# Optimization experiments

Measured on AMD Instinct MI355X. Metric: run time of the kernel, lower is better.

Reference implementation:

```python
import jax, jax.numpy as jnp
import numpy as np
import math

B, H, S, D = 2, 16, 2048, 128
COEFF = 2.0  # layer_number


def setup_inputs() -> dict:
    key = jax.random.key(0)
    kq, kk, kv = jax.random.split(key, 3)
    return {
        "query_layer": jax.random.normal(kq, (B, H, S, D), dtype=jnp.float32),
        "key_layer": jax.random.normal(kk, (B, H, S, D), dtype=jnp.float32),
        "value_layer": jax.random.normal(kv, (B, H, S, D), dtype=jnp.float32),
    }


def reference(query_layer, key_layer, value_layer):
    b, h, sq, d = query_layer.shape
    sk = key_layer.shape[2]
    norm_factor = math.sqrt(d) * COEFF
    # raw scores [b,h,sq,sk]; divide by sqrt(d)*coeff, cast fp32, multiply by coeff
    scores = jnp.einsum("bhqd,bhkd->bhqk", query_layer, key_layer) / norm_factor
    scores = scores.astype(jnp.float32) * COEFF
    # causal mask (sq == sk path with attention_mask=None)
    causal = jnp.tril(jnp.ones((sq, sk), dtype=bool))
    scores = jnp.where(causal, scores, jnp.float32(-jnp.inf))
    probs = jax.nn.softmax(scores, axis=-1).astype(value_layer.dtype)
    # dropout p=0.0 -> identity
    ctx = jnp.einsum("bhqk,bhkd->bhqd", probs, value_layer)
    # [b,h,sq,d] -> [b,sq,h*d]
    return ctx.transpose(0, 2, 1, 3).reshape(b, sq, h * d)
```

## Files before the change

### kernel.cpp

```cpp
#include <hip/hip_runtime.h>
#include <hip/hip_bf16.h>
#include <math.h>

#define NB 2
#define NH 16
#define NS 2048
#define ND 128

typedef __bf16 bf16x8 __attribute__((ext_vector_type(8)));
typedef __bf16 bf16x4 __attribute__((ext_vector_type(4)));
typedef float f32x4 __attribute__((ext_vector_type(4)));

#define KTILE 64
#define KSTR 136
#define VSTR 72
#define PSTR 72


__global__ __launch_bounds__(256, 2)
void fa_fwd(const float* __restrict__ Qg_, const float* __restrict__ Kg_,
            const float* __restrict__ Vg_, float* __restrict__ Out)
{
    __shared__ __bf16 Kl[KTILE][KSTR];
    __shared__ __bf16 Vt[ND + 16][VSTR];
    __shared__ __bf16 Pl[4][16][PSTR];

    const int tid  = threadIdx.x;
    const int w    = tid >> 6;
    const int lane = tid & 63;
    const int quad = lane >> 4;
    const int l15  = lane & 15;

    const int pr = blockIdx.x >> 5;
    const int bh = blockIdx.x & 31;
    const int b  = bh >> 4;
    const int h  = bh & 15;
    const int qtA = 31 - pr, qtB = pr;
    const int ntA = qtA + 1;
    const int total = ntA + qtB + 1;

    const float* Qg = Qg_ + (size_t)bh * NS * ND;
    const float* Kg = Kg_ + (size_t)bh * NS * ND;
    const float* Vg = Vg_ + (size_t)bh * NS * ND;

    for (int i = tid; i < 16*VSTR; i += 256) {
        int r = i / VSTR, c = i - r*VSTR;
        Vt[ND + r][c] = (r == 0) ? (__bf16)1.0f : (__bf16)0.0f;
    }

    const float CSC = 0.08838834764831845f * 1.4426950408889634f;

    bf16x8 qfA[4], qfB[4];
    const int qA = qtA * 64, qB = qtB * 64;
    {
        const float* qp = Qg + (size_t)(qA + 16*w + l15) * ND + quad*8;
        #pragma unroll
        for (int ks = 0; ks < 4; ++ks) {
            float4 a = *(const float4*)(qp + ks*32);
            float4 c = *(const float4*)(qp + ks*32 + 4);
            bf16x8 f;
            f[0]=(__bf16)(a.x*CSC); f[1]=(__bf16)(a.y*CSC); f[2]=(__bf16)(a.z*CSC); f[3]=(__bf16)(a.w*CSC);
            f[4]=(__bf16)(c.x*CSC); f[5]=(__bf16)(c.y*CSC); f[6]=(__bf16)(c.z*CSC); f[7]=(__bf16)(c.w*CSC);
            qfA[ks] = f;
        }
        const float* qp2 = Qg + (size_t)(qB + 16*w + l15) * ND + quad*8;
        #pragma unroll
        for (int ks = 0; ks < 4; ++ks) {
            float4 a = *(const float4*)(qp2 + ks*32);
            float4 c = *(const float4*)(qp2 + ks*32 + 4);
            bf16x8 f;
            f[0]=(__bf16)(a.x*CSC); f[1]=(__bf16)(a.y*CSC); f[2]=(__bf16)(a.z*CSC); f[3]=(__bf16)(a.w*CSC);
            f[4]=(__bf16)(c.x*CSC); f[5]=(__bf16)(c.y*CSC); f[6]=(__bf16)(c.z*CSC); f[7]=(__bf16)(c.w*CSC);
            qfB[ks] = f;
        }
    }
    bf16x8 qcur[4];
    #pragma unroll
    for (int ks = 0; ks < 4; ++ks) qcur[ks] = qfA[ks];

    f32x4 O[9];
    #pragma unroll
    for (int dt = 0; dt < 9; ++dt)
        #pragma unroll
        for (int r = 0; r < 4; ++r) O[dt][r] = 0.0f;

    float4 kp[8];
    float  vp[32];
    const int vc = tid & 127;
    const int vh = tid >> 7;

    {
        #pragma unroll
        for (int i = 0; i < 8; ++i)
            kp[i] = *(const float4*)(Kg + ((i*256 + tid) << 2));
        const float* vs = Vg + (size_t)(vh*32) * ND + vc;
        #pragma unroll
        for (int i = 0; i < 32; ++i) vp[i] = vs[i*ND];
    }

    for (int t = 0; t < total; ++t) {
        const int phase = (t >= ntA);
        const int jt  = phase ? t - ntA : t;
        const int kv0 = jt * KTILE;
        __syncthreads();

        #pragma unroll
        for (int i = 0; i < 8; ++i) {
            int idx = (i*256 + tid) << 2;
            int r = idx >> 7, c = idx & 127;
            bf16x4 f; f[0]=(__bf16)kp[i].x; f[1]=(__bf16)kp[i].y; f[2]=(__bf16)kp[i].z; f[3]=(__bf16)kp[i].w;
            *(bf16x4*)&Kl[r][c] = f;
        }
        #pragma unroll
        for (int g = 0; g < 4; ++g) {
            bf16x8 f;
            #pragma unroll
            for (int j = 0; j < 8; ++j) f[j] = (__bf16)vp[g*8 + j];
            *(bf16x8*)&Vt[vc][vh*32 + g*8] = f;
        }

        if (t + 1 < total) {
            const int jt2 = (t + 1 >= ntA) ? t + 1 - ntA : t + 1;
            const int kv1 = jt2 * KTILE;
            const float* ks2 = Kg + (size_t)kv1 * ND;
            #pragma unroll
            for (int i = 0; i < 8; ++i)
                kp[i] = *(const float4*)(ks2 + ((i*256 + tid) << 2));
            const float* vs = Vg + (size_t)(kv1 + vh*32) * ND + vc;
            #pragma unroll
            for (int i = 0; i < 32; ++i) vp[i] = vs[i*ND];
        }

        __syncthreads();

        if (t == ntA) {
            #pragma unroll
            for (int r = 0; r < 4; ++r) {
                float lsum = __shfl(O[8][r], lane & 48, 64);
                float inv = 1.0f / lsum;
                int q = qA + 16*w + quad*4 + r;
                float* op = Out + ((size_t)(b*NS + q)) * (NH*ND) + h*ND + l15;
                #pragma unroll
                for (int dt = 0; dt < 8; ++dt)
                    op[dt*16] = O[dt][r] * inv;
            }
            #pragma unroll
            for (int dt = 0; dt < 9; ++dt)
                #pragma unroll
                for (int r = 0; r < 4; ++r) O[dt][r] = 0.0f;
            #pragma unroll
            for (int ks = 0; ks < 4; ++ks) qcur[ks] = qfB[ks];
        }

        const int qb  = (phase ? qB : qA) + 16*w;
        const bool diag = (jt == (phase ? qtB : qtA));

        f32x4 Sf[4];
        #pragma unroll
        for (int n = 0; n < 4; ++n)
            #pragma unroll
            for (int r = 0; r < 4; ++r) Sf[n][r] = 0.0f;
        #pragma unroll
        for (int ks = 0; ks < 4; ++ks) {
            bf16x8 bf[4];
            #pragma unroll
            for (int n = 0; n < 4; ++n)
                bf[n] = *(const bf16x8*)&Kl[n*16 + l15][ks*32 + quad*8];
            #pragma unroll
            for (int n = 0; n < 4; ++n)
                Sf[n] = __builtin_amdgcn_mfma_f32_16x16x32_bf16(qcur[ks], bf[n], Sf[n], 0, 0, 0);
        }

        #pragma unroll
        for (int n = 0; n < 4; ++n) {
            const int kg = kv0 + n*16 + l15;
            #pragma unroll
            for (int r = 0; r < 4; ++r) {
                float tv = Sf[n][r];
                if (diag) {
                    int qg = qb + quad*4 + r;
                    if (kg > qg) tv = -INFINITY;
                }
                Pl[w][r*4 + quad][n*16 + l15] = (__bf16)exp2f(tv);
            }
        }

        #pragma unroll
        for (int ks = 0; ks < 2; ++ks) {
            bf16x8 af = *(const bf16x8*)&Pl[w][((l15 & 3) << 2) | (l15 >> 2)][ks*32 + quad*8];
            #pragma unroll
            for (int dt = 0; dt < 9; ++dt) {
                bf16x8 vf = *(const bf16x8*)&Vt[dt*16 + l15][ks*32 + quad*8];
                O[dt] = __builtin_amdgcn_mfma_f32_16x16x32_bf16(af, vf, O[dt], 0, 0, 0);
            }
        }
    }

    #pragma unroll
    for (int r = 0; r < 4; ++r) {
        float lsum = __shfl(O[8][r], lane & 48, 64);
        float inv = 1.0f / lsum;
        int q = qB + 16*w + quad*4 + r;
        float* op = Out + ((size_t)(b*NS + q)) * (NH*ND) + h*ND + l15;
        #pragma unroll
        for (int dt = 0; dt < 8; ++dt)
            op[dt*16] = O[dt][r] * inv;
    }
}

extern "C" void kernel_launch(void* const* d_in, const int* in_sizes, int n_in,
                              void* d_out, int out_size, void* d_ws, size_t ws_size,
                              hipStream_t stream) {
    const float* Q = (const float*)d_in[0];
    const float* K = (const float*)d_in[1];
    const float* V = (const float*)d_in[2];
    float* Out = (float*)d_out;
    dim3 grid(512);
    fa_fwd<<<grid, dim3(256), 0, stream>>>(Q, K, V, Out);
}
```

Baseline: 202.4 us.

## Pre-convert K/V to swizzled bf16 tiles and stream via async LDS loads

A new prep kernel converts K and V to bf16 once, writing per-tile XOR-swizzled layouts, with V stored transposed, into the workspace. The attention kernel then double-buffers those tiles into LDS with global_load_lds direct copies instead of register-staged fp32 loads and in-kernel conversion. It also swaps the MFMA operand order so P lands in LDS without a transpose, and replaces the ones-column row-sum trick with a register accumulator reduced by shuffles. This removes repeated fp32 K/V conversion per query tile and frees the extra MFMA column, at the cost of an extra kernel launch and a workspace round trip.

```diff
diff --git a/kernel.cpp b/kernel.cpp
--- a/kernel.cpp
+++ b/kernel.cpp
@@ -11,19 +11,52 @@
 typedef __bf16 bf16x4 __attribute__((ext_vector_type(4)));
 typedef float f32x4 __attribute__((ext_vector_type(4)));
 
-#define KTILE 64
-#define KSTR 136
-#define VSTR 72
-#define PSTR 72
-
+__global__ __launch_bounds__(256)
+void prep(const float* __restrict__ K, const float* __restrict__ V,
+          char* __restrict__ Kb, char* __restrict__ Vb)
+{
+    int g = blockIdx.x * 256 + threadIdx.x;
+    if (g < (1 << 20)) {
+        const int c8 = g & 15;
+        const int row = g >> 4;
+        const int s = row & 2047, bh = row >> 11;
+        const int jt = s >> 6, r = s & 63;
+        const float* src = K + ((size_t)row << 7) + (c8 << 3);
+        float4 a = *(const float4*)src;
+        float4 c = *(const float4*)(src + 4);
+        bf16x8 o;
+        o[0]=(__bf16)a.x; o[1]=(__bf16)a.y; o[2]=(__bf16)a.z; o[3]=(__bf16)a.w;
+        o[4]=(__bf16)c.x; o[5]=(__bf16)c.y; o[6]=(__bf16)c.z; o[7]=(__bf16)c.w;
+        *(bf16x8*)(Kb + (((size_t)(bh*32 + jt)) << 14) + r*256 + ((c8 ^ (r & 7)) << 4)) = o;
+    } else {
+        g -= (1 << 20);
+        const int t   = g >> 10;
+        const int off = g & 1023;
+        const int d = off >> 3, sl = off & 7;
+        const int g8 = sl ^ (d & 7);
+        const int bh = t >> 5, jt = t & 31;
+        const float* src = V + (((size_t)(bh*2048 + jt*64 + g8*8)) << 7) + d;
+        bf16x8 o;
+        #pragma unroll
+        for (int j = 0; j < 8; ++j) o[j] = (__bf16)src[(size_t)j << 7];
+        *(bf16x8*)(Vb + (((size_t)t) << 14) + d*128 + (sl << 4)) = o;
+    }
+}
+
+__device__ __forceinline__ void gld16(void* lds, const void* gsrc)
+{
+    __builtin_amdgcn_global_load_lds(
+        (const __attribute__((address_space(1))) void*)gsrc,
+        (__attribute__((address_space(3))) void*)lds, 16, 0, 0);
+}
 
 __global__ __launch_bounds__(256, 2)
-void fa_fwd(const float* __restrict__ Qg_, const float* __restrict__ Kg_,
-            const float* __restrict__ Vg_, float* __restrict__ Out)
+void fa_fwd(const float* __restrict__ Qg_, const char* __restrict__ Kb,
+            const char* __restrict__ Vb, float* __restrict__ Out)
 {
-    __shared__ __bf16 Kl[KTILE][KSTR];
-    __shared__ __bf16 Vt[ND + 16][VSTR];
-    __shared__ __bf16 Pl[4][16][PSTR];
+    __shared__ __bf16 Kl[2][8192];
+    __shared__ __bf16 Vl[2][8192];
+    __shared__ __bf16 Pl[4][1024];
 
     const int tid  = threadIdx.x;
     const int w    = tid >> 6;
@@ -33,27 +66,23 @@
 
     const int pr = blockIdx.x >> 5;
     const int bh = blockIdx.x & 31;
-    const int b  = bh >> 4;
-    const int h  = bh & 15;
+    const int b  = bh >> 4, h = bh & 15;
     const int qtA = 31 - pr, qtB = pr;
     const int ntA = qtA + 1;
     const int total = ntA + qtB + 1;
+    const int qA = qtA * 64, qB = qtB * 64;
 
     const float* Qg = Qg_ + (size_t)bh * NS * ND;
-    const float* Kg = Kg_ + (size_t)bh * NS * ND;
-    const float* Vg = Vg_ + (size_t)bh * NS * ND;
-
-    for (int i = tid; i < 16*VSTR; i += 256) {
-        int r = i / VSTR, c = i - r*VSTR;
-        Vt[ND + r][c] = (r == 0) ? (__bf16)1.0f : (__bf16)0.0f;
-    }
+    const char*  Kt = Kb + ((size_t)bh << 19);
+    const char*  Vt = Vb + ((size_t)bh << 19);
+
+    const int xo = (l15 & 7) << 4;
 
     const float CSC = 0.08838834764831845f * 1.4426950408889634f;
-
-    bf16x8 qfA[4], qfB[4];
-    const int qA = qtA * 64, qB = qtB * 64;
+    bf16x8 qfA[4], qfB[4], qcur[4];
     {
-        const float* qp = Qg + (size_t)(qA + 16*w + l15) * ND + quad*8;
+        const float* qp  = Qg + (size_t)(qA + 16*w + l15) * ND + quad*8;
+        const float* qp2 = Qg + (size_t)(qB + 16*w + l15) * ND + quad*8;
         #pragma unroll
         for (int ks = 0; ks < 4; ++ks) {
             float4 a = *(const float4*)(qp + ks*32);
@@ -62,99 +91,84 @@
             f[0]=(__bf16)(a.x*CSC); f[1]=(__bf16)(a.y*CSC); f[2]=(__bf16)(a.z*CSC); f[3]=(__bf16)(a.w*CSC);
             f[4]=(__bf16)(c.x*CSC); f[5]=(__bf16)(c.y*CSC); f[6]=(__bf16)(c.z*CSC); f[7]=(__bf16)(c.w*CSC);
             qfA[ks] = f;
-        }
-        const float* qp2 = Qg + (size_t)(qB + 16*w + l15) * ND + quad*8;
-        #pragma unroll
-        for (int ks = 0; ks < 4; ++ks) {
-            float4 a = *(const float4*)(qp2 + ks*32);
-            float4 c = *(const float4*)(qp2 + ks*32 + 4);
-            bf16x8 f;
-            f[0]=(__bf16)(a.x*CSC); f[1]=(__bf16)(a.y*CSC); f[2]=(__bf16)(a.z*CSC); f[3]=(__bf16)(a.w*CSC);
-            f[4]=(__bf16)(c.x*CSC); f[5]=(__bf16)(c.y*CSC); f[6]=(__bf16)(c.z*CSC); f[7]=(__bf16)(c.w*CSC);
-            qfB[ks] = f;
+            float4 a2 = *(const float4*)(qp2 + ks*32);
+            float4 c2 = *(const float4*)(qp2 + ks*32 + 4);
+            bf16x8 f2;
+            f2[0]=(__bf16)(a2.x*CSC); f2[1]=(__bf16)(a2.y*CSC); f2[2]=(__bf16)(a2.z*CSC); f2[3]=(__bf16)(a2.w*CSC);
+            f2[4]=(__bf16)(c2.x*CSC); f2[5]=(__bf16)(c2.y*CSC); f2[6]=(__bf16)(c2.z*CSC); f2[7]=(__bf16)(c2.w*CSC);
+            qfB[ks] = f2;
         }
     }
-    bf16x8 qcur[4];
     #pragma unroll
     for (int ks = 0; ks < 4; ++ks) qcur[ks] = qfA[ks];
 
-    f32x4 O[9];
+    f32x4 O[8];
     #pragma unroll
-    for (int dt = 0; dt < 9; ++dt)
+    for (int dt = 0; dt < 8; ++dt)
         #pragma unroll
         for (int r = 0; r < 4; ++r) O[dt][r] = 0.0f;
-
-    float4 kp[8];
-    float  vp[32];
-    const int vc = tid & 127;
-    const int vh = tid >> 7;
-
-    {
-        #pragma unroll
-        for (int i = 0; i < 8; ++i)
-            kp[i] = *(const float4*)(Kg + ((i*256 + tid) << 2));
-        const float* vs = Vg + (size_t)(vh*32) * ND + vc;
-        #pragma unroll
-        for (int i = 0; i < 32; ++i) vp[i] = vs[i*ND];
-    }
+    float rs = 0.0f;
+
+    char* const klds0 = (char*)&Kl[0][0];
+    char* const vlds0 = (char*)&Vl[0][0];
+    char* const Pw    = (char*)&Pl[w][0];
+
+    auto stage = [&](int jt, int buf) {
+        const char* kg = Kt + (((size_t)jt) << 14) + w*4096 + lane*16;
+        const char* vg = Vt + (((size_t)jt) << 14) + w*4096 + lane*16;
+        char* kl = klds0 + buf*16384 + w*4096;
+        char* vl = vlds0 + buf*16384 + w*4096;
+        #pragma unroll
+        for (int i = 0; i < 4; ++i) {
+            gld16(kl + i*1024, kg + i*1024);
+            gld16(vl + i*1024, vg + i*1024);
+        }
+    };
+
+    auto flush = [&](int qb) {
+        float s1 = rs + __shfl_xor(rs, 16, 64);
+        float s2 = s1 + __shfl_xor(s1, 32, 64);
+        #pragma unroll
+        for (int r = 0; r < 4; ++r) {
+            float lsum = __shfl(s2, quad*4 + r, 64);
+            float inv = 1.0f / lsum;
+            int q = qb + 16*w + quad*4 + r;
+            float* op = Out + ((size_t)(b*NS + q)) * (NH*ND) + h*ND + l15;
+            #pragma unroll
+            for (int dt = 0; dt < 8; ++dt)
+                op[dt*16] = O[dt][r] * inv;
+        }
+    };
+
+    stage(0, 0);
+    int cur = 0;
 
     for (int t = 0; t < total; ++t) {
         const int phase = (t >= ntA);
-        const int jt  = phase ? t - ntA : t;
-        const int kv0 = jt * KTILE;
-        __syncthreads();
-
-        #pragma unroll
-        for (int i = 0; i < 8; ++i) {
-            int idx = (i*256 + tid) << 2;
-            int r = idx >> 7, c = idx & 127;
-            bf16x4 f; f[0]=(__bf16)kp[i].x; f[1]=(__bf16)kp[i].y; f[2]=(__bf16)kp[i].z; f[3]=(__bf16)kp[i].w;
-            *(bf16x4*)&Kl[r][c] = f;
-        }
-        #pragma unroll
-        for (int g = 0; g < 4; ++g) {
-            bf16x8 f;
-            #pragma unroll
-            for (int j = 0; j < 8; ++j) f[j] = (__bf16)vp[g*8 + j];
-            *(bf16x8*)&Vt[vc][vh*32 + g*8] = f;
-        }
+        const bool diag = (phase ? (t - ntA) == qtB : t == qtA);
 
         if (t + 1 < total) {
-            const int jt2 = (t + 1 >= ntA) ? t + 1 - ntA : t + 1;
-            const int kv1 = jt2 * KTILE;
-            const float* ks2 = Kg + (size_t)kv1 * ND;
-            #pragma unroll
-            for (int i = 0; i < 8; ++i)
-                kp[i] = *(const float4*)(ks2 + ((i*256 + tid) << 2));
-            const float* vs = Vg + (size_t)(kv1 + vh*32) * ND + vc;
-            #pragma unroll
-            for (int i = 0; i < 32; ++i) vp[i] = vs[i*ND];
-        }
-
-        __syncthreads();
+            const int jt2 = (t + 1 >= ntA) ? (t + 1 - ntA) : (t + 1);
+            stage(jt2, cur ^ 1);
+            asm volatile("s_waitcnt vmcnt(8)" ::: "memory");
+        } else {
+            asm volatile("s_waitcnt vmcnt(0)" ::: "memory");
+        }
+        __builtin_amdgcn_s_barrier();
+        asm volatile("" ::: "memory");
 
         if (t == ntA) {
-            #pragma unroll
-            for (int r = 0; r < 4; ++r) {
-                float lsum = __shfl(O[8][r], lane & 48, 64);
-                float inv = 1.0f / lsum;
-                int q = qA + 16*w + quad*4 + r;
-                float* op = Out + ((size_t)(b*NS + q)) * (NH*ND) + h*ND + l15;
-                #pragma unroll
-                for (int dt = 0; dt < 8; ++dt)
-                    op[dt*16] = O[dt][r] * inv;
-            }
-            #pragma unroll
-            for (int dt = 0; dt < 9; ++dt)
+            flush(qA);
+            rs = 0.0f;
+            #pragma unroll
+            for (int dt = 0; dt < 8; ++dt)
                 #pragma unroll
                 for (int r = 0; r < 4; ++r) O[dt][r] = 0.0f;
             #pragma unroll
             for (int ks = 0; ks < 4; ++ks) qcur[ks] = qfB[ks];
         }
 
-        const int qb  = (phase ? qB : qA) + 16*w;
-        const bool diag = (jt == (phase ? qtB : qtA));
-
+        const char* Kc = klds0 + cur*16384;
         f32x4 Sf[4];
         #pragma unroll
         for (int n = 0; n < 4; ++n)
@@ -162,50 +176,48 @@
             for (int r = 0; r < 4; ++r) Sf[n][r] = 0.0f;
         #pragma unroll
         for (int ks = 0; ks < 4; ++ks) {
-            bf16x8 bf[4];
+            bf16x8 kf[4];
             #pragma unroll
             for (int n = 0; n < 4; ++n)
-                bf[n] = *(const bf16x8*)&Kl[n*16 + l15][ks*32 + quad*8];
+                kf[n] = *(const bf16x8*)(Kc + (n*16 + l15)*256 + ((((ks*4 + quad) << 4)) ^ xo));
             #pragma unroll
             for (int n = 0; n < 4; ++n)
-                Sf[n] = __builtin_amdgcn_mfma_f32_16x16x32_bf16(qcur[ks], bf[n], Sf[n], 0, 0, 0);
+                Sf[n] = __builtin_amdgcn_mfma_f32_16x16x32_bf16(kf[n], qcur[ks], Sf[n], 0, 0, 0);
         }
 
         #pragma unroll
         for (int n = 0; n < 4; ++n) {
-            const int kg = kv0 + n*16 + l15;
+            bf16x4 pk;
             #pragma unroll
             for (int r = 0; r < 4; ++r) {
-                float tv = Sf[n][r];
+                float e = exp2f(Sf[n][r]);
                 if (diag) {
-                    int qg = qb + quad*4 + r;
-                    if (kg > qg) tv = -INFINITY;
+                    int kvg = n*16 + quad*4 + r;
+                    int qg  = 16*w + l15;
+                    if (kvg > qg) e = 0.0f;
                 }
-                Pl[w][r*4 + quad][n*16 + l15] = (__bf16)exp2f(tv);
+                pk[r] = (__bf16)e;
+                rs += (float)pk[r];
             }
-        }
-
+            *(bf16x4*)(Pw + l15*128 + ((((n*2 + (quad >> 1)) << 4)) ^ xo) + ((quad & 1) << 3)) = pk;
+        }
+
+        const char* Vc = vlds0 + cur*16384;
         #pragma unroll
         for (int ks = 0; ks < 2; ++ks) {
-            bf16x8 af = *(const bf16x8*)&Pl[w][((l15 & 3) << 2) | (l15 >> 2)][ks*32 + quad*8];
-            #pragma unroll
-            for (int dt = 0; dt < 9; ++dt) {
-                bf16x8 vf = *(const bf16x8*)&Vt[dt*16 + l15][ks*32 + quad*8];
-                O[dt] = __builtin_amdgcn_mfma_f32_16x16x32_bf16(af, vf, O[dt], 0, 0, 0);
+            bf16x8 pa = *(const bf16x8*)(Pw + l15*128 + ((((ks*4 + quad) << 4)) ^ xo));
+            #pragma unroll
+            for (int dt = 0; dt < 8; ++dt) {
+                bf16x8 vf = *(const bf16x8*)(Vc + (dt*16 + l15)*128 + ((((ks*4 + quad) << 4)) ^ xo));
+                O[dt] = __builtin_amdgcn_mfma_f32_16x16x32_bf16(pa, vf, O[dt], 0, 0, 0);
             }
         }
+
+        __syncthreads();
+        cur ^= 1;
     }
 
-    #pragma unroll
-    for (int r = 0; r < 4; ++r) {
-        float lsum = __shfl(O[8][r], lane & 48, 64);
-        float inv = 1.0f / lsum;
-        int q = qB + 16*w + quad*4 + r;
-        float* op = Out + ((size_t)(b*NS + q)) * (NH*ND) + h*ND + l15;
-        #pragma unroll
-        for (int dt = 0; dt < 8; ++dt)
-            op[dt*16] = O[dt][r] * inv;
-    }
+    flush(qB);
 }
 
 extern "C" void kernel_launch(void* const* d_in, const int* in_sizes, int n_in,
@@ -215,6 +227,8 @@
     const float* K = (const float*)d_in[1];
     const float* V = (const float*)d_in[2];
     float* Out = (float*)d_out;
-    dim3 grid(512);
-    fa_fwd<<<grid, dim3(256), 0, stream>>>(Q, K, V, Out);
-}
+    char* Kb = (char*)d_ws;
+    char* Vb = (char*)d_ws + ((size_t)32 << 19);
+    prep<<<dim3(8192), dim3(256), 0, stream>>>(K, V, Kb, Vb);
+    fa_fwd<<<dim3(512), dim3(256), 0, stream>>>(Q, Kb, Vb, Out);
+}
```

Result: faster. 192.2 us (-5.0%).
